# Kernel optimization log

Hardware: AMD Instinct MI355X
Metric: run time of the kernel (lower is better)

## Reference

```python
import jax, jax.numpy as jnp
import numpy as np

N_NODES = 50000
N_EDGES = 800000
D_MODEL = 128
N_HEADS = 8
HEAD_DIM = D_MODEL // N_HEADS
SCALE = 1.0 / np.sqrt(HEAD_DIM)


def _linear_params(key, d_in, d_out):
    kw, kb = jax.random.split(key)
    bound = 1.0 / np.sqrt(d_in)
    W = jax.random.uniform(kw, (d_in, d_out), jnp.float32, -bound, bound)
    b = jax.random.uniform(kb, (d_out,), jnp.float32, -bound, bound)
    return W, b


def setup_inputs() -> dict:
    key = jax.random.key(0)
    ks = jax.random.split(key, 8)
    node_features = jax.random.normal(ks[0], (N_NODES, D_MODEL), jnp.float32)
    edge_index = jax.random.randint(ks[1], (2, N_EDGES), 0, N_NODES, jnp.int64 if jax.config.jax_enable_x64 else jnp.int32)
    edge_features = jax.random.normal(ks[2], (N_EDGES, D_MODEL), jnp.float32)
    Wq, bq = _linear_params(ks[3], D_MODEL, D_MODEL)
    Wk, bk = _linear_params(ks[4], D_MODEL, D_MODEL)
    Wv, bv = _linear_params(ks[5], D_MODEL, D_MODEL)
    We, be = _linear_params(ks[6], D_MODEL, N_HEADS)
    Wo, bo = _linear_params(ks[7], D_MODEL, D_MODEL)
    return {"node_features": node_features, "edge_index": edge_index,
            "edge_features": edge_features,
            "Wq": Wq, "bq": bq, "Wk": Wk, "bk": bk, "Wv": Wv, "bv": bv,
            "We": We, "be": be, "Wo": Wo, "bo": bo}


def reference(node_features, edge_index, edge_features,
              Wq, bq, Wk, bk, Wv, bv, We, be, Wo, bo):
    N = node_features.shape[0]
    Q = (node_features @ Wq + bq).reshape(N, N_HEADS, HEAD_DIM)
    K = (node_features @ Wk + bk).reshape(N, N_HEADS, HEAD_DIM)
    V = (node_features @ Wv + bv).reshape(N, N_HEADS, HEAD_DIM)
    row, col = edge_index[0], edge_index[1]
    # edge scores: [E, H]
    scores = jnp.einsum('ehd,ehd->eh', Q[row], K[col]) * SCALE
    scores = scores + (edge_features @ We + be)
    # segment softmax over destination node (row), per head
    seg_max = jax.ops.segment_max(scores, row, num_segments=N)          # [N, H]
    seg_max = jnp.where(jnp.isfinite(seg_max), seg_max, 0.0)
    ex = jnp.exp(scores - seg_max[row])                                  # [E, H]
    denom = jax.ops.segment_sum(ex, row, num_segments=N)                 # [N, H]
    att = ex / denom[row]
    # weighted aggregate of neighbor values: [N, H, D]
    out = jax.ops.segment_sum(att[:, :, None] * V[col], row, num_segments=N)
    out = out.reshape(N, D_MODEL)
    return out @ Wo + bo
```

## Files before the change

### kernel.cpp

```cpp
#include <hip/hip_runtime.h>
#include <hip/hip_bf16.h>
#include <math.h>

#define NNODES 50000
#define NEDGES 800000
#define DMODEL 128
#define QK_SCALE 0.25f
#define NSB 196
#define KVROW 384

typedef float fvec4 __attribute__((ext_vector_type(4)));
typedef float fvec2 __attribute__((ext_vector_type(2)));
typedef short sv8  __attribute__((ext_vector_type(8)));

__device__ __forceinline__ unsigned short f2bf(float f) {
    unsigned int u = __float_as_uint(f);
    unsigned int r = (u + 0x7FFFu + ((u >> 16) & 1u)) >> 16;
    return (unsigned short)r;
}

__device__ __forceinline__ void bf8_to_f32(uint4 u, fvec4& lo, fvec4& hi) {
    lo.x = __uint_as_float(u.x << 16); lo.y = __uint_as_float(u.x & 0xFFFF0000u);
    lo.z = __uint_as_float(u.y << 16); lo.w = __uint_as_float(u.y & 0xFFFF0000u);
    hi.x = __uint_as_float(u.z << 16); hi.y = __uint_as_float(u.z & 0xFFFF0000u);
    hi.z = __uint_as_float(u.w << 16); hi.w = __uint_as_float(u.w & 0xFFFF0000u);
}

__device__ __forceinline__ void fp8x4_to_f32(unsigned int u, fvec4& k) {
    fvec2 lo = __builtin_amdgcn_cvt_pk_f32_fp8(u, false);
    fvec2 hi = __builtin_amdgcn_cvt_pk_f32_fp8(u, true);
    k.x = lo.x; k.y = lo.y; k.z = hi.x; k.w = hi.y;
}

__device__ __forceinline__ unsigned char f2fp8(float v) {
    unsigned int pk = (unsigned int)__builtin_amdgcn_cvt_pk_fp8_f32(v, v, 0, false);
    return (unsigned char)(pk & 0xFFu);
}

__global__ __launch_bounds__(256) void prep_kernel(const float* __restrict__ X,
                                                   const float* __restrict__ Wq,
                                                   const float* __restrict__ Wk,
                                                   const float* __restrict__ Wv,
                                                   const float* __restrict__ Wo,
                                                   unsigned short* __restrict__ Xb,
                                                   unsigned short* __restrict__ Wb,
                                                   int* __restrict__ cnt) {
    int i = blockIdx.x * 256 + threadIdx.x;
    if (i < NNODES * 32) {
        float4 v = *(const float4*)&X[(size_t)i * 4];
        ushort4 s;
        s.x = f2bf(v.x); s.y = f2bf(v.y); s.z = f2bf(v.z); s.w = f2bf(v.w);
        *(ushort4*)&Xb[(size_t)i * 4] = s;
    } else {
        int j = i - NNODES * 32;
        if (j < 4 * 16384) {
            int w = j >> 14, rem = j & 16383;
            int n = rem >> 7, k = rem & 127;
            const float* src = (w == 0) ? Wq : (w == 1) ? Wk : (w == 2) ? Wv : Wo;
            Wb[j] = f2bf(src[k * 128 + n]);
        } else {
            int c = j - 4 * 16384;
            if (c < NNODES) cnt[c] = 0;
        }
    }
}

__global__ __launch_bounds__(256) void gemm_qkv(const unsigned short* __restrict__ Xb,
                                                const unsigned short* __restrict__ Wb,
                                                const float* __restrict__ bq,
                                                const float* __restrict__ bk,
                                                const float* __restrict__ bv,
                                                unsigned short* __restrict__ Qb,
                                                unsigned char* __restrict__ KVb,
                                                int M) {
    __shared__ unsigned short Als[64 * 128];
    __shared__ unsigned short Bls[128 * 128];
    char* Ac = (char*)Als;
    char* Bc = (char*)Bls;

    int z = blockIdx.y;
    int r0 = blockIdx.x * 64;
    int tid = threadIdx.x;
    int wave = tid >> 6, lane = tid & 63;

    const char* Wsrc = (const char*)(Wb + (size_t)z * 16384);

    #pragma unroll
    for (int p = 0; p < 4; ++p) {
        int o = p * 4096 + tid * 16;
        int r = o >> 8;
        int gr = r0 + r; if (gr >= M) gr = M - 1;
        uint4 v = *(const uint4*)((const char*)Xb + (size_t)gr * 256 + (o & 255));
        *(uint4*)(Ac + r * 256 + ((o & 255) ^ ((r & 7) << 4))) = v;
    }
    #pragma unroll
    for (int p = 0; p < 8; ++p) {
        int o = p * 4096 + tid * 16;
        int r = o >> 8;
        uint4 v = *(const uint4*)(Wsrc + o);
        *(uint4*)(Bc + (o ^ ((r & 7) << 4))) = v;
    }
    __syncthreads();

    fvec4 acc[8] = {};
    int arow = wave * 16 + (lane & 15);
    int kchunk = (lane >> 4) * 16;

    #pragma unroll
    for (int ks = 0; ks < 4; ++ks) {
        int ain = (ks * 64 + kchunk) ^ ((arow & 7) << 4);
        sv8 af = *(const sv8*)(Ac + arow * 256 + ain);
        #pragma unroll
        for (int cf = 0; cf < 8; ++cf) {
            int brow = cf * 16 + (lane & 15);
            int bin = (ks * 64 + kchunk) ^ ((brow & 7) << 4);
            sv8 bf = *(const sv8*)(Bc + brow * 256 + bin);
            acc[cf] = __builtin_amdgcn_mfma_f32_16x16x32_bf16(af, bf, acc[cf], 0, 0, 0);
        }
    }

    const float* bias = (z == 0) ? bq : (z == 1) ? bk : bv;

    #pragma unroll
    for (int cf = 0; cf < 8; ++cf) {
        int col = cf * 16 + (lane & 15);
        float b = bias[col];
        #pragma unroll
        for (int r = 0; r < 4; ++r) {
            int gr = r0 + wave * 16 + ((lane >> 4) * 4) + r;
            if (gr < M) {
                float val = acc[cf][r] + b;
                if (z == 0) {
                    Qb[(size_t)gr * 128 + col] = f2bf(val);
                } else if (z == 1) {
                    KVb[(size_t)gr * KVROW + col] = f2fp8(val);
                } else {
                    int boff = 128 + ((col & 8) << 4) + ((col >> 4) << 4) + ((col & 7) << 1);
                    *(unsigned short*)(KVb + (size_t)gr * KVROW + boff) = f2bf(val);
                }
            }
        }
    }
}

__global__ __launch_bounds__(256) void gemm_out(const unsigned short* __restrict__ Ab,
                                                const unsigned short* __restrict__ Wob,
                                                const float* __restrict__ bo,
                                                float* __restrict__ outp, int M) {
    __shared__ unsigned short Als[64 * 128];
    __shared__ unsigned short Bls[128 * 128];
    char* Ac = (char*)Als;
    char* Bc = (char*)Bls;

    int r0 = blockIdx.x * 64;
    int tid = threadIdx.x;
    int wave = tid >> 6, lane = tid & 63;

    #pragma unroll
    for (int p = 0; p < 4; ++p) {
        int o = p * 4096 + tid * 16;
        int r = o >> 8;
        int gr = r0 + r; if (gr >= M) gr = M - 1;
        uint4 v = *(const uint4*)((const char*)Ab + (size_t)gr * 256 + (o & 255));
        *(uint4*)(Ac + r * 256 + ((o & 255) ^ ((r & 7) << 4))) = v;
    }
    #pragma unroll
    for (int p = 0; p < 8; ++p) {
        int o = p * 4096 + tid * 16;
        int r = o >> 8;
        uint4 v = *(const uint4*)((const char*)Wob + o);
        *(uint4*)(Bc + (o ^ ((r & 7) << 4))) = v;
    }
    __syncthreads();

    fvec4 acc[8] = {};
    int arow = wave * 16 + (lane & 15);
    int kchunk = (lane >> 4) * 16;

    #pragma unroll
    for (int ks = 0; ks < 4; ++ks) {
        int ain = (ks * 64 + kchunk) ^ ((arow & 7) << 4);
        sv8 af = *(const sv8*)(Ac + arow * 256 + ain);
        #pragma unroll
        for (int cf = 0; cf < 8; ++cf) {
            int brow = cf * 16 + (lane & 15);
            int bin = (ks * 64 + kchunk) ^ ((brow & 7) << 4);
            sv8 bf = *(const sv8*)(Bc + brow * 256 + bin);
            acc[cf] = __builtin_amdgcn_mfma_f32_16x16x32_bf16(af, bf, acc[cf], 0, 0, 0);
        }
    }

    #pragma unroll
    for (int cf = 0; cf < 8; ++cf) {
        int col = cf * 16 + (lane & 15);
        float b = bo[col];
        #pragma unroll
        for (int r = 0; r < 4; ++r) {
            int gr = r0 + wave * 16 + ((lane >> 4) * 4) + r;
            if (gr < M) outp[(size_t)gr * 128 + col] = acc[cf][r] + b;
        }
    }
}

__global__ __launch_bounds__(256) void hist_kernel(const int* __restrict__ row,
                                                   int* __restrict__ cnt) {
    int e = blockIdx.x * 256 + threadIdx.x;
    if (e < NEDGES) atomicAdd(&cnt[row[e]], 1);
}

__global__ __launch_bounds__(256) void scan1_kernel(const int* __restrict__ cnt,
                                                    int* __restrict__ bsum) {
    __shared__ int red[256];
    int idx = blockIdx.x * 256 + threadIdx.x;
    red[threadIdx.x] = (idx < NNODES) ? cnt[idx] : 0;
    __syncthreads();
    for (int off = 128; off > 0; off >>= 1) {
        if (threadIdx.x < off) red[threadIdx.x] += red[threadIdx.x + off];
        __syncthreads();
    }
    if (threadIdx.x == 0) bsum[blockIdx.x] = red[0];
}

__global__ __launch_bounds__(256) void scan2_kernel(const int* __restrict__ bsum,
                                                    int* __restrict__ bpre) {
    __shared__ int ps[256];
    int t = threadIdx.x;
    int v = (t < NSB) ? bsum[t] : 0;
    ps[t] = v;
    __syncthreads();
    for (int off = 1; off < 256; off <<= 1) {
        int x = (t >= off) ? ps[t - off] : 0;
        __syncthreads();
        ps[t] += x;
        __syncthreads();
    }
    if (t < NSB) bpre[t] = ps[t] - v;
}

__global__ __launch_bounds__(256) void scan3_kernel(const int* __restrict__ cnt,
                                                    const int* __restrict__ bpre,
                                                    int* __restrict__ offs,
                                                    int* __restrict__ cursor) {
    __shared__ int ps[256];
    int t = threadIdx.x;
    int idx = blockIdx.x * 256 + t;
    int v = (idx < NNODES) ? cnt[idx] : 0;
    ps[t] = v;
    __syncthreads();
    for (int off = 1; off < 256; off <<= 1) {
        int x = (t >= off) ? ps[t - off] : 0;
        __syncthreads();
        ps[t] += x;
        __syncthreads();
    }
    int ex = ps[t] - v + bpre[blockIdx.x];
    if (idx < NNODES) { offs[idx] = ex; cursor[idx] = ex; }
    if (idx == NNODES) offs[NNODES] = NEDGES;
}

__global__ __launch_bounds__(256) void ef_bias_scatter(const float* __restrict__ EF,
                                                       const int* __restrict__ row,
                                                       const int* __restrict__ col,
                                                       int* __restrict__ cursor,
                                                       const float* __restrict__ We,
                                                       const float* __restrict__ be,
                                                       unsigned short* __restrict__ ebias,
                                                       int* __restrict__ col_perm) {
    __shared__ float sWe[8][128];
    __shared__ float sbe[8];
    for (int i = threadIdx.x; i < 1024; i += 256) {
        int d = i >> 3, h = i & 7;
        sWe[h][d] = We[i];
    }
    if (threadIdx.x < 8) sbe[threadIdx.x] = be[threadIdx.x];
    __syncthreads();

    int g = blockIdx.x * 256 + threadIdx.x;
    int e = g >> 3;
    int s = g & 7;
    if (e >= NEDGES) return;
    int lane = threadIdx.x & 63;

    int pos = 0;
    if (s == 0) {
        int r = row[e];
        pos = atomicAdd(&cursor[r], 1);
        col_perm[pos] = col[e];
    }

    const fvec4* efv = (const fvec4*)(EF + (size_t)e * 128);
    float acc[8] = {0.f, 0.f, 0.f, 0.f, 0.f, 0.f, 0.f, 0.f};
    #pragma unroll
    for (int i = 0; i < 4; ++i) {
        int d4 = s + 8 * i;
        fvec4 v = __builtin_nontemporal_load(&efv[d4]);
        #pragma unroll
        for (int h = 0; h < 8; ++h) {
            fvec4 w = *(const fvec4*)&sWe[h][d4 * 4];
            acc[h] += v.x * w.x + v.y * w.y + v.z * w.z + v.w * w.w;
        }
    }

    #pragma unroll
    for (int off = 1; off < 8; off <<= 1)
        #pragma unroll
        for (int h = 0; h < 8; ++h)
            acc[h] += __shfl_xor(acc[h], off);

    pos = __shfl(pos, lane & ~7);
    ebias[(size_t)pos * 8 + s] = f2bf(acc[s] + sbe[s]);
}

__global__ __launch_bounds__(256) void fused_agg(const unsigned short* __restrict__ Qb,
                                                 const unsigned char* __restrict__ KV,
                                                 const unsigned short* __restrict__ ebias,
                                                 const int* __restrict__ col_perm,
                                                 const int* __restrict__ offs,
                                                 unsigned short* __restrict__ aggb) {
    int node = blockIdx.x * 4 + (threadIdx.x >> 6);
    if (node >= NNODES) return;
    int lane = threadIdx.x & 63;
    int slot = lane >> 3;
    int h    = lane & 7;
    int start = offs[node];
    int end   = offs[node + 1];

    const uint4* qp = (const uint4*)(Qb + (size_t)node * 128 + h * 16);
    uint4 qu0 = qp[0], qu1 = qp[1];
    fvec4 q0, q1, q2, q3;
    bf8_to_f32(qu0, q0, q1);
    bf8_to_f32(qu1, q2, q3);

    float m = -3.0e38f;
    float sum = 0.0f;
    fvec4 a0 = {0.f,0.f,0.f,0.f}, a1 = {0.f,0.f,0.f,0.f};
    fvec4 a2 = {0.f,0.f,0.f,0.f}, a3 = {0.f,0.f,0.f,0.f};

    int i = start + slot;
    int c = (i < end) ? col_perm[i] : 0;
    for (; i < end; i += 8) {
        int c_next = (i + 8 < end) ? col_perm[i + 8] : 0;
        float eb = __uint_as_float(((unsigned int)ebias[(size_t)i * 8 + h]) << 16);
        const uint4* kp = (const uint4*)(KV + (size_t)c * KVROW);
        uint4 ku  = kp[h];
        uint4 vu0 = kp[8 + h];
        uint4 vu1 = kp[16 + h];
        fvec4 k0, k1, k2, k3, v0, v1, v2, v3;
        fp8x4_to_f32(ku.x, k0);
        fp8x4_to_f32(ku.y, k1);
        fp8x4_to_f32(ku.z, k2);
        fp8x4_to_f32(ku.w, k3);
        bf8_to_f32(vu0, v0, v1);
        bf8_to_f32(vu1, v2, v3);

        fvec4 d4 = q0 * k0 + q1 * k1 + q2 * k2 + q3 * k3;
        float dot = d4.x + d4.y + d4.z + d4.w;

        float s = dot * QK_SCALE + eb;
        float mn = fmaxf(m, s);
        float corr = __expf(m - mn);
        float w = __expf(s - mn);
        sum = sum * corr + w;
        a0 = a0 * corr + w * v0;
        a1 = a1 * corr + w * v1;
        a2 = a2 * corr + w * v2;
        a3 = a3 * corr + w * v3;
        m = mn;
        c = c_next;
    }

    #pragma unroll
    for (int off = 8; off < 64; off <<= 1) {
        float mo = __shfl_xor(m, off);
        float so = __shfl_xor(sum, off);
        fvec4 b0, b1, b2, b3;
        b0.x = __shfl_xor(a0.x, off); b0.y = __shfl_xor(a0.y, off);
        b0.z = __shfl_xor(a0.z, off); b0.w = __shfl_xor(a0.w, off);
        b1.x = __shfl_xor(a1.x, off); b1.y = __shfl_xor(a1.y, off);
        b1.z = __shfl_xor(a1.z, off); b1.w = __shfl_xor(a1.w, off);
        b2.x = __shfl_xor(a2.x, off); b2.y = __shfl_xor(a2.y, off);
        b2.z = __shfl_xor(a2.z, off); b2.w = __shfl_xor(a2.w, off);
        b3.x = __shfl_xor(a3.x, off); b3.y = __shfl_xor(a3.y, off);
        b3.z = __shfl_xor(a3.z, off); b3.w = __shfl_xor(a3.w, off);
        float M = fmaxf(m, mo);
        float c1 = __expf(m - M);
        float c2 = __expf(mo - M);
        sum = sum * c1 + so * c2;
        a0 = a0 * c1 + b0 * c2;
        a1 = a1 * c1 + b1 * c2;
        a2 = a2 * c1 + b2 * c2;
        a3 = a3 * c1 + b3 * c2;
        m = M;
    }

    if (slot == 0) {
        float inv = (sum > 0.0f) ? (1.0f / sum) : 0.0f;
        unsigned short* op = aggb + (size_t)node * 128 + h * 16;
        ushort4 s;
        s.x = f2bf(a0.x * inv); s.y = f2bf(a0.y * inv); s.z = f2bf(a0.z * inv); s.w = f2bf(a0.w * inv);
        *(ushort4*)(op + 0) = s;
        s.x = f2bf(a1.x * inv); s.y = f2bf(a1.y * inv); s.z = f2bf(a1.z * inv); s.w = f2bf(a1.w * inv);
        *(ushort4*)(op + 4) = s;
        s.x = f2bf(a2.x * inv); s.y = f2bf(a2.y * inv); s.z = f2bf(a2.z * inv); s.w = f2bf(a2.w * inv);
        *(ushort4*)(op + 8) = s;
        s.x = f2bf(a3.x * inv); s.y = f2bf(a3.y * inv); s.z = f2bf(a3.z * inv); s.w = f2bf(a3.w * inv);
        *(ushort4*)(op + 12) = s;
    }
}

extern "C" void kernel_launch(void* const* d_in, const int* in_sizes, int n_in,
                              void* d_out, int out_size, void* d_ws, size_t ws_size,
                              hipStream_t stream) {
    const float* node = (const float*)d_in[0];
    const int*   ei   = (const int*)d_in[1];
    const float* ef   = (const float*)d_in[2];
    const float* Wq   = (const float*)d_in[3];
    const float* bq   = (const float*)d_in[4];
    const float* Wk   = (const float*)d_in[5];
    const float* bk   = (const float*)d_in[6];
    const float* Wv   = (const float*)d_in[7];
    const float* bv   = (const float*)d_in[8];
    const float* We   = (const float*)d_in[9];
    const float* be   = (const float*)d_in[10];
    const float* Wo   = (const float*)d_in[11];
    const float* bo   = (const float*)d_in[12];
    float* out = (float*)d_out;

    const int* row = ei;
    const int* col = ei + NEDGES;

    unsigned short* Qb   = (unsigned short*)d_ws;
    unsigned char*  KVb  = (unsigned char*)(Qb + (size_t)NNODES * 128);
    unsigned short* Xb   = (unsigned short*)(KVb + (size_t)NNODES * KVROW);
    unsigned short* Wb   = Xb  + (size_t)NNODES * 128;
    unsigned short* aggb = Wb  + 4 * 16384;
    unsigned short* ebb  = aggb + (size_t)NNODES * 128;
    int*   cnt      = (int*)(ebb + (size_t)NEDGES * 8);
    int*   offs     = cnt + NNODES;
    int*   cursor   = offs + NNODES + 1;
    int*   col_perm = cursor + NNODES;
    int*   bsum     = col_perm + NEDGES;
    int*   bpre     = bsum + 256;

    prep_kernel<<<(NNODES * 32 + 4 * 16384 + NNODES + 255) / 256, 256, 0, stream>>>(
        node, Wq, Wk, Wv, Wo, Xb, Wb, cnt);
    hist_kernel<<<(NEDGES + 255) / 256, 256, 0, stream>>>(row, cnt);
    scan1_kernel<<<NSB, 256, 0, stream>>>(cnt, bsum);
    scan2_kernel<<<1, 256, 0, stream>>>(bsum, bpre);
    scan3_kernel<<<NSB, 256, 0, stream>>>(cnt, bpre, offs, cursor);

    dim3 gqkv((NNODES + 63) / 64, 3);
    gemm_qkv<<<gqkv, 256, 0, stream>>>(Xb, Wb, bq, bk, bv, Qb, KVb, NNODES);

    ef_bias_scatter<<<NEDGES * 8 / 256, 256, 0, stream>>>(ef, row, col, cursor, We, be, ebb, col_perm);

    fused_agg<<<(NNODES + 3) / 4, 256, 0, stream>>>(Qb, KVb, ebb, col_perm, offs, aggb);

    gemm_out<<<(NNODES + 63) / 64, 256, 0, stream>>>(aggb, Wb + 3 * 16384, bo, out, NNODES);
}
```

Measured before the change: 304.7 us.

## Fuse edge-bias projection into aggregation and overlap edge scatter with QKV GEMM

Removes the separate edge-feature bias kernel: the CSR scatter now runs as an extra grid slice of the QKV GEMM kernel and records an edge permutation, and the aggregation kernel reads each edge's features via that permutation and computes the per-head bias inline with shared-memory weights and shuffles. This eliminates a kernel launch and the intermediate bias buffer write and read. In exchange, edge features are gathered in permuted rather than sequential order, and the aggregation loop gains substantial per-edge ALU, LDS and shuffle work on its critical path.

```diff
diff --git a/kernel.cpp b/kernel.cpp
--- a/kernel.cpp
+++ b/kernel.cpp
@@ -72,13 +72,28 @@
                                                 const float* __restrict__ bv,
                                                 unsigned short* __restrict__ Qb,
                                                 unsigned char* __restrict__ KVb,
+                                                const int* __restrict__ row,
+                                                const int* __restrict__ col,
+                                                int* __restrict__ cursor,
+                                                int* __restrict__ col_perm,
+                                                int* __restrict__ e_perm,
                                                 int M) {
     __shared__ unsigned short Als[64 * 128];
     __shared__ unsigned short Bls[128 * 128];
+
+    int z = blockIdx.y;
+    if (z == 3) {
+        int stride = gridDim.x * 256;
+        for (int e = blockIdx.x * 256 + threadIdx.x; e < NEDGES; e += stride) {
+            int pos = atomicAdd(&cursor[row[e]], 1);
+            col_perm[pos] = col[e];
+            e_perm[pos]   = e;
+        }
+        return;
+    }
+
     char* Ac = (char*)Als;
     char* Bc = (char*)Bls;
-
-    int z = blockIdx.y;
     int r0 = blockIdx.x * 64;
     int tid = threadIdx.x;
     int wave = tid >> 6, lane = tid & 63;
@@ -123,19 +138,19 @@
 
     #pragma unroll
     for (int cf = 0; cf < 8; ++cf) {
-        int col = cf * 16 + (lane & 15);
-        float b = bias[col];
+        int col_ = cf * 16 + (lane & 15);
+        float b = bias[col_];
         #pragma unroll
         for (int r = 0; r < 4; ++r) {
             int gr = r0 + wave * 16 + ((lane >> 4) * 4) + r;
             if (gr < M) {
                 float val = acc[cf][r] + b;
                 if (z == 0) {
-                    Qb[(size_t)gr * 128 + col] = f2bf(val);
+                    Qb[(size_t)gr * 128 + col_] = f2bf(val);
                 } else if (z == 1) {
-                    KVb[(size_t)gr * KVROW + col] = f2fp8(val);
+                    KVb[(size_t)gr * KVROW + col_] = f2fp8(val);
                 } else {
-                    int boff = 128 + ((col & 8) << 4) + ((col >> 4) << 4) + ((col & 7) << 1);
+                    int boff = 128 + ((col_ & 8) << 4) + ((col_ >> 4) << 4) + ((col_ & 7) << 1);
                     *(unsigned short*)(KVb + (size_t)gr * KVROW + boff) = f2bf(val);
                 }
             }
@@ -258,65 +273,24 @@
     if (idx == NNODES) offs[NNODES] = NEDGES;
 }
 
-__global__ __launch_bounds__(256) void ef_bias_scatter(const float* __restrict__ EF,
-                                                       const int* __restrict__ row,
-                                                       const int* __restrict__ col,
-                                                       int* __restrict__ cursor,
-                                                       const float* __restrict__ We,
-                                                       const float* __restrict__ be,
-                                                       unsigned short* __restrict__ ebias,
-                                                       int* __restrict__ col_perm) {
+__global__ __launch_bounds__(256) void fused_agg(const unsigned short* __restrict__ Qb,
+                                                 const unsigned char* __restrict__ KV,
+                                                 const float* __restrict__ EF,
+                                                 const int* __restrict__ col_perm,
+                                                 const int* __restrict__ e_perm,
+                                                 const int* __restrict__ offs,
+                                                 const float* __restrict__ We,
+                                                 const float* __restrict__ be,
+                                                 unsigned short* __restrict__ aggb) {
     __shared__ float sWe[8][128];
     __shared__ float sbe[8];
-    for (int i = threadIdx.x; i < 1024; i += 256) {
-        int d = i >> 3, h = i & 7;
-        sWe[h][d] = We[i];
+    for (int t = threadIdx.x; t < 1024; t += 256) {
+        int d = t >> 3, hh = t & 7;
+        sWe[hh][d] = We[t];
     }
     if (threadIdx.x < 8) sbe[threadIdx.x] = be[threadIdx.x];
     __syncthreads();
 
-    int g = blockIdx.x * 256 + threadIdx.x;
-    int e = g >> 3;
-    int s = g & 7;
-    if (e >= NEDGES) return;
-    int lane = threadIdx.x & 63;
-
-    int pos = 0;
-    if (s == 0) {
-        int r = row[e];
-        pos = atomicAdd(&cursor[r], 1);
-        col_perm[pos] = col[e];
-    }
-
-    const fvec4* efv = (const fvec4*)(EF + (size_t)e * 128);
-    float acc[8] = {0.f, 0.f, 0.f, 0.f, 0.f, 0.f, 0.f, 0.f};
-    #pragma unroll
-    for (int i = 0; i < 4; ++i) {
-        int d4 = s + 8 * i;
-        fvec4 v = __builtin_nontemporal_load(&efv[d4]);
-        #pragma unroll
-        for (int h = 0; h < 8; ++h) {
-            fvec4 w = *(const fvec4*)&sWe[h][d4 * 4];
-            acc[h] += v.x * w.x + v.y * w.y + v.z * w.z + v.w * w.w;
-        }
-    }
-
-    #pragma unroll
-    for (int off = 1; off < 8; off <<= 1)
-        #pragma unroll
-        for (int h = 0; h < 8; ++h)
-            acc[h] += __shfl_xor(acc[h], off);
-
-    pos = __shfl(pos, lane & ~7);
-    ebias[(size_t)pos * 8 + s] = f2bf(acc[s] + sbe[s]);
-}
-
-__global__ __launch_bounds__(256) void fused_agg(const unsigned short* __restrict__ Qb,
-                                                 const unsigned char* __restrict__ KV,
-                                                 const unsigned short* __restrict__ ebias,
-                                                 const int* __restrict__ col_perm,
-                                                 const int* __restrict__ offs,
-                                                 unsigned short* __restrict__ aggb) {
     int node = blockIdx.x * 4 + (threadIdx.x >> 6);
     if (node >= NNODES) return;
     int lane = threadIdx.x & 63;
@@ -331,20 +305,30 @@
     bf8_to_f32(qu0, q0, q1);
     bf8_to_f32(qu1, q2, q3);
 
+    float be_h = sbe[h];
+
     float m = -3.0e38f;
     float sum = 0.0f;
     fvec4 a0 = {0.f,0.f,0.f,0.f}, a1 = {0.f,0.f,0.f,0.f};
     fvec4 a2 = {0.f,0.f,0.f,0.f}, a3 = {0.f,0.f,0.f,0.f};
 
     int i = start + slot;
-    int c = (i < end) ? col_perm[i] : 0;
+    int c = 0, e = 0;
+    if (i < end) { c = col_perm[i]; e = e_perm[i]; }
     for (; i < end; i += 8) {
-        int c_next = (i + 8 < end) ? col_perm[i + 8] : 0;
-        float eb = __uint_as_float(((unsigned int)ebias[(size_t)i * 8 + h]) << 16);
+        int c_next = 0, e_next = 0;
+        if (i + 8 < end) { c_next = col_perm[i + 8]; e_next = e_perm[i + 8]; }
+
         const uint4* kp = (const uint4*)(KV + (size_t)c * KVROW);
         uint4 ku  = kp[h];
         uint4 vu0 = kp[8 + h];
         uint4 vu1 = kp[16 + h];
+        const fvec4* efv = (const fvec4*)(EF + (size_t)e * 128);
+        fvec4 f0 = __builtin_nontemporal_load(&efv[h]);
+        fvec4 f1 = __builtin_nontemporal_load(&efv[h + 8]);
+        fvec4 f2 = __builtin_nontemporal_load(&efv[h + 16]);
+        fvec4 f3 = __builtin_nontemporal_load(&efv[h + 24]);
+
         fvec4 k0, k1, k2, k3, v0, v1, v2, v3;
         fp8x4_to_f32(ku.x, k0);
         fp8x4_to_f32(ku.y, k1);
@@ -355,6 +339,34 @@
 
         fvec4 d4 = q0 * k0 + q1 * k1 + q2 * k2 + q3 * k3;
         float dot = d4.x + d4.y + d4.z + d4.w;
+
+        float p0, p1, p2, p3, p4, p5, p6, p7;
+        {
+            int d0 = (h + 0)  * 4;
+            int d1 = (h + 8)  * 4;
+            int d2 = (h + 16) * 4;
+            int d3 = (h + 24) * 4;
+            #define EFW(hh, pv) { \
+                fvec4 w0 = *(const fvec4*)&sWe[hh][d0]; \
+                fvec4 w1 = *(const fvec4*)&sWe[hh][d1]; \
+                fvec4 w2 = *(const fvec4*)&sWe[hh][d2]; \
+                fvec4 w3 = *(const fvec4*)&sWe[hh][d3]; \
+                fvec4 t = f0 * w0 + f1 * w1 + f2 * w2 + f3 * w3; \
+                pv = t.x + t.y + t.z + t.w; }
+            EFW(0, p0) EFW(1, p1) EFW(2, p2) EFW(3, p3)
+            EFW(4, p4) EFW(5, p5) EFW(6, p6) EFW(7, p7)
+            #undef EFW
+        }
+        #pragma unroll
+        for (int off = 1; off < 8; off <<= 1) {
+            p0 += __shfl_xor(p0, off); p1 += __shfl_xor(p1, off);
+            p2 += __shfl_xor(p2, off); p3 += __shfl_xor(p3, off);
+            p4 += __shfl_xor(p4, off); p5 += __shfl_xor(p5, off);
+            p6 += __shfl_xor(p6, off); p7 += __shfl_xor(p7, off);
+        }
+        float eb = (h < 4) ? ((h < 2) ? (h == 0 ? p0 : p1) : (h == 2 ? p2 : p3))
+                           : ((h < 6) ? (h == 4 ? p4 : p5) : (h == 6 ? p6 : p7));
+        eb += be_h;
 
         float s = dot * QK_SCALE + eb;
         float mn = fmaxf(m, s);
@@ -366,7 +378,7 @@
         a2 = a2 * corr + w * v2;
         a3 = a3 * corr + w * v3;
         m = mn;
-        c = c_next;
+        c = c_next; e = e_next;
     }
 
     #pragma unroll
@@ -434,12 +446,12 @@
     unsigned short* Xb   = (unsigned short*)(KVb + (size_t)NNODES * KVROW);
     unsigned short* Wb   = Xb  + (size_t)NNODES * 128;
     unsigned short* aggb = Wb  + 4 * 16384;
-    unsigned short* ebb  = aggb + (size_t)NNODES * 128;
-    int*   cnt      = (int*)(ebb + (size_t)NEDGES * 8);
+    int*   cnt      = (int*)(aggb + (size_t)NNODES * 128);
     int*   offs     = cnt + NNODES;
     int*   cursor   = offs + NNODES + 1;
     int*   col_perm = cursor + NNODES;
-    int*   bsum     = col_perm + NEDGES;
+    int*   e_perm   = col_perm + NEDGES;
+    int*   bsum     = e_perm + NEDGES;
     int*   bpre     = bsum + 256;
 
     prep_kernel<<<(NNODES * 32 + 4 * 16384 + NNODES + 255) / 256, 256, 0, stream>>>(
@@ -449,12 +461,12 @@
     scan2_kernel<<<1, 256, 0, stream>>>(bsum, bpre);
     scan3_kernel<<<NSB, 256, 0, stream>>>(cnt, bpre, offs, cursor);
 
-    dim3 gqkv((NNODES + 63) / 64, 3);
-    gemm_qkv<<<gqkv, 256, 0, stream>>>(Xb, Wb, bq, bk, bv, Qb, KVb, NNODES);
-
-    ef_bias_scatter<<<NEDGES * 8 / 256, 256, 0, stream>>>(ef, row, col, cursor, We, be, ebb, col_perm);
-
-    fused_agg<<<(NNODES + 3) / 4, 256, 0, stream>>>(Qb, KVb, ebb, col_perm, offs, aggb);
+    dim3 gqkv((NNODES + 63) / 64, 4);
+    gemm_qkv<<<gqkv, 256, 0, stream>>>(Xb, Wb, bq, bk, bv, Qb, KVb,
+                                       row, col, cursor, col_perm, e_perm, NNODES);
+
+    fused_agg<<<(NNODES + 3) / 4, 256, 0, stream>>>(Qb, KVb, ef, col_perm, e_perm,
+                                                    offs, We, be, aggb);
 
     gemm_out<<<(NNODES + 63) / 64, 256, 0, stream>>>(aggb, Wb + 3 * 16384, bo, out, NNODES);
 }
```

Measured after the change: 367.7 us. 1.21x slower.

## Compute full edge scores in scatter kernel and drop K reads from aggregation

Applied to the files above, without the earlier changes.

Moves the Q·K dot-product out of the per-node aggregation loop and into the edge scatter kernel, which now gathers Q[row] and K[col] per edge, adds the edge bias, and writes the full fp32 score in CSR order. The aggregation kernel then reads only the precomputed score and V, which shortens its dependent gather chain and drops its col prefetch. In exchange the scatter kernel does an extra random gather of Q and K per edge, and the score buffer grows from bf16 to fp32 (doubling that write and read traffic).

```diff
diff --git a/kernel.cpp b/kernel.cpp
--- a/kernel.cpp
+++ b/kernel.cpp
@@ -123,19 +123,19 @@
 
     #pragma unroll
     for (int cf = 0; cf < 8; ++cf) {
-        int col = cf * 16 + (lane & 15);
-        float b = bias[col];
+        int col_ = cf * 16 + (lane & 15);
+        float b = bias[col_];
         #pragma unroll
         for (int r = 0; r < 4; ++r) {
             int gr = r0 + wave * 16 + ((lane >> 4) * 4) + r;
             if (gr < M) {
                 float val = acc[cf][r] + b;
                 if (z == 0) {
-                    Qb[(size_t)gr * 128 + col] = f2bf(val);
+                    Qb[(size_t)gr * 128 + col_] = f2bf(val);
                 } else if (z == 1) {
-                    KVb[(size_t)gr * KVROW + col] = f2fp8(val);
+                    KVb[(size_t)gr * KVROW + col_] = f2fp8(val);
                 } else {
-                    int boff = 128 + ((col & 8) << 4) + ((col >> 4) << 4) + ((col & 7) << 1);
+                    int boff = 128 + ((col_ & 8) << 4) + ((col_ >> 4) << 4) + ((col_ & 7) << 1);
                     *(unsigned short*)(KVb + (size_t)gr * KVROW + boff) = f2bf(val);
                 }
             }
@@ -258,14 +258,16 @@
     if (idx == NNODES) offs[NNODES] = NEDGES;
 }
 
-__global__ __launch_bounds__(256) void ef_bias_scatter(const float* __restrict__ EF,
-                                                       const int* __restrict__ row,
-                                                       const int* __restrict__ col,
-                                                       int* __restrict__ cursor,
-                                                       const float* __restrict__ We,
-                                                       const float* __restrict__ be,
-                                                       unsigned short* __restrict__ ebias,
-                                                       int* __restrict__ col_perm) {
+__global__ __launch_bounds__(256) void score_scatter(const float* __restrict__ EF,
+                                                     const int* __restrict__ row,
+                                                     const int* __restrict__ col,
+                                                     int* __restrict__ cursor,
+                                                     const float* __restrict__ We,
+                                                     const float* __restrict__ be,
+                                                     const unsigned short* __restrict__ Qb,
+                                                     const unsigned char* __restrict__ KVb,
+                                                     float* __restrict__ scores,
+                                                     int* __restrict__ col_perm) {
     __shared__ float sWe[8][128];
     __shared__ float sbe[8];
     for (int i = threadIdx.x; i < 1024; i += 256) {
@@ -281,12 +283,18 @@
     if (e >= NEDGES) return;
     int lane = threadIdx.x & 63;
 
+    int r = row[e];
+    int c = col[e];
+
     int pos = 0;
     if (s == 0) {
-        int r = row[e];
         pos = atomicAdd(&cursor[r], 1);
-        col_perm[pos] = col[e];
-    }
+        col_perm[pos] = c;
+    }
+
+    const uint4* qp = (const uint4*)(Qb + (size_t)r * 128 + s * 16);
+    uint4 qu0 = qp[0], qu1 = qp[1];
+    uint4 ku = *(const uint4*)(KVb + (size_t)c * KVROW + s * 16);
 
     const fvec4* efv = (const fvec4*)(EF + (size_t)e * 128);
     float acc[8] = {0.f, 0.f, 0.f, 0.f, 0.f, 0.f, 0.f, 0.f};
@@ -307,13 +315,22 @@
         for (int h = 0; h < 8; ++h)
             acc[h] += __shfl_xor(acc[h], off);
 
+    fvec4 q0, q1, q2, q3, k0, k1, k2, k3;
+    bf8_to_f32(qu0, q0, q1);
+    bf8_to_f32(qu1, q2, q3);
+    fp8x4_to_f32(ku.x, k0);
+    fp8x4_to_f32(ku.y, k1);
+    fp8x4_to_f32(ku.z, k2);
+    fp8x4_to_f32(ku.w, k3);
+    fvec4 d4v = q0 * k0 + q1 * k1 + q2 * k2 + q3 * k3;
+    float dot = d4v.x + d4v.y + d4v.z + d4v.w;
+
     pos = __shfl(pos, lane & ~7);
-    ebias[(size_t)pos * 8 + s] = f2bf(acc[s] + sbe[s]);
-}
-
-__global__ __launch_bounds__(256) void fused_agg(const unsigned short* __restrict__ Qb,
+    scores[(size_t)pos * 8 + s] = dot * QK_SCALE + acc[s] + sbe[s];
+}
+
+__global__ __launch_bounds__(256) void fused_agg(const float* __restrict__ scores,
                                                  const unsigned char* __restrict__ KV,
-                                                 const unsigned short* __restrict__ ebias,
                                                  const int* __restrict__ col_perm,
                                                  const int* __restrict__ offs,
                                                  unsigned short* __restrict__ aggb) {
@@ -325,38 +342,21 @@
     int start = offs[node];
     int end   = offs[node + 1];
 
-    const uint4* qp = (const uint4*)(Qb + (size_t)node * 128 + h * 16);
-    uint4 qu0 = qp[0], qu1 = qp[1];
-    fvec4 q0, q1, q2, q3;
-    bf8_to_f32(qu0, q0, q1);
-    bf8_to_f32(qu1, q2, q3);
-
     float m = -3.0e38f;
     float sum = 0.0f;
     fvec4 a0 = {0.f,0.f,0.f,0.f}, a1 = {0.f,0.f,0.f,0.f};
     fvec4 a2 = {0.f,0.f,0.f,0.f}, a3 = {0.f,0.f,0.f,0.f};
 
-    int i = start + slot;
-    int c = (i < end) ? col_perm[i] : 0;
-    for (; i < end; i += 8) {
-        int c_next = (i + 8 < end) ? col_perm[i + 8] : 0;
-        float eb = __uint_as_float(((unsigned int)ebias[(size_t)i * 8 + h]) << 16);
+    for (int i = start + slot; i < end; i += 8) {
+        int c = col_perm[i];
+        float s = scores[(size_t)i * 8 + h];
         const uint4* kp = (const uint4*)(KV + (size_t)c * KVROW);
-        uint4 ku  = kp[h];
         uint4 vu0 = kp[8 + h];
         uint4 vu1 = kp[16 + h];
-        fvec4 k0, k1, k2, k3, v0, v1, v2, v3;
-        fp8x4_to_f32(ku.x, k0);
-        fp8x4_to_f32(ku.y, k1);
-        fp8x4_to_f32(ku.z, k2);
-        fp8x4_to_f32(ku.w, k3);
+        fvec4 v0, v1, v2, v3;
         bf8_to_f32(vu0, v0, v1);
         bf8_to_f32(vu1, v2, v3);
 
-        fvec4 d4 = q0 * k0 + q1 * k1 + q2 * k2 + q3 * k3;
-        float dot = d4.x + d4.y + d4.z + d4.w;
-
-        float s = dot * QK_SCALE + eb;
         float mn = fmaxf(m, s);
         float corr = __expf(m - mn);
         float w = __expf(s - mn);
@@ -366,7 +366,6 @@
         a2 = a2 * corr + w * v2;
         a3 = a3 * corr + w * v3;
         m = mn;
-        c = c_next;
     }
 
     #pragma unroll
@@ -434,8 +433,8 @@
     unsigned short* Xb   = (unsigned short*)(KVb + (size_t)NNODES * KVROW);
     unsigned short* Wb   = Xb  + (size_t)NNODES * 128;
     unsigned short* aggb = Wb  + 4 * 16384;
-    unsigned short* ebb  = aggb + (size_t)NNODES * 128;
-    int*   cnt      = (int*)(ebb + (size_t)NEDGES * 8);
+    float* scores  = (float*)(aggb + (size_t)NNODES * 128);
+    int*   cnt      = (int*)(scores + (size_t)NEDGES * 8);
     int*   offs     = cnt + NNODES;
     int*   cursor   = offs + NNODES + 1;
     int*   col_perm = cursor + NNODES;
@@ -452,9 +451,10 @@
     dim3 gqkv((NNODES + 63) / 64, 3);
     gemm_qkv<<<gqkv, 256, 0, stream>>>(Xb, Wb, bq, bk, bv, Qb, KVb, NNODES);
 
-    ef_bias_scatter<<<NEDGES * 8 / 256, 256, 0, stream>>>(ef, row, col, cursor, We, be, ebb, col_perm);
-
-    fused_agg<<<(NNODES + 3) / 4, 256, 0, stream>>>(Qb, KVb, ebb, col_perm, offs, aggb);
+    score_scatter<<<NEDGES * 8 / 256, 256, 0, stream>>>(ef, row, col, cursor, We, be,
+                                                        Qb, KVb, scores, col_perm);
+
+    fused_agg<<<(NNODES + 3) / 4, 256, 0, stream>>>(scores, KVb, col_perm, offs, aggb);
 
     gemm_out<<<(NNODES + 63) / 64, 256, 0, stream>>>(aggb, Wb + 3 * 16384, bo, out, NNODES);
 }
```

New measurement: 279.9 us (median of 2 runs). -8.1%, faster.
